# Optimization experiments

Hardware: AMD Instinct MI355X
Metric: run time of the kernel (lower is better)

The kernel has to match this reference:

```python
import jax, jax.numpy as jnp
import numpy as np

N_NODES = 100000
N_EDGES = 1600000
IN_CH = 128
HID = 64
OUT_CH = 10
N_GRAPHS = 64
NEG_SLOPE = 0.2   # GATv2Conv default negative_slope
EPS = 1e-16       # PyG softmax eps


def setup_inputs() -> dict:
    key = jax.random.key(0)
    ks = jax.random.split(key, 10)
    x = jax.random.normal(ks[0], (N_NODES, IN_CH), dtype=jnp.float32)
    edge_index = jax.random.randint(ks[1], (2, N_EDGES), 0, N_NODES, dtype=jnp.int64)
    batch = jnp.sort(jax.random.randint(ks[2], (N_NODES,), 0, N_GRAPHS, dtype=jnp.int64))
    s = 1.0 / np.sqrt(IN_CH)
    Wl = jax.random.uniform(ks[3], (IN_CH, HID), jnp.float32, -s, s)   # lin_l (source)
    Wr = jax.random.uniform(ks[4], (IN_CH, HID), jnp.float32, -s, s)   # lin_r (target)
    att = jax.random.uniform(ks[5], (HID,), jnp.float32, -1.0 / np.sqrt(HID), 1.0 / np.sqrt(HID))
    bias = jnp.zeros((HID,), jnp.float32)
    sf = 1.0 / np.sqrt(HID)
    fc_w = jax.random.uniform(ks[6], (HID, OUT_CH), jnp.float32, -sf, sf)
    fc_b = jax.random.uniform(ks[7], (OUT_CH,), jnp.float32, -sf, sf)
    return {"x": x, "Wl": Wl, "Wr": Wr, "att": att, "bias": bias,
            "fc_w": fc_w, "fc_b": fc_b, "edge_index": edge_index, "batch": batch}


def reference(x, Wl, Wr, att, bias, fc_w, fc_b, edge_index, batch):
    src, tgt = edge_index[0], edge_index[1]
    # GATv2Conv, heads=1: separate linear for source/target
    xl = x @ Wl                         # [N, H] messages (source side)
    xr = x @ Wr                         # [N, H] target side
    z = xl[src] + xr[tgt]               # [E, H]
    e = jnp.where(z > 0, z, NEG_SLOPE * z) @ att   # [E]
    # segment softmax over incoming edges of each target node
    m = jax.ops.segment_max(e, tgt, num_segments=N_NODES)      # [N]
    a = jnp.exp(e - m[tgt])                                    # [E]
    denom = jax.ops.segment_sum(a, tgt, num_segments=N_NODES)  # [N]
    alpha = a / (denom[tgt] + EPS)                             # [E]
    out = jax.ops.segment_sum(alpha[:, None] * xl[src], tgt, num_segments=N_NODES)
    out = out + bias                                           # [N, H]
    # global mean pool over graphs
    cnt = jax.ops.segment_sum(jnp.ones((N_NODES,), out.dtype), batch, num_segments=N_GRAPHS)
    pooled = jax.ops.segment_sum(out, batch, num_segments=N_GRAPHS) / jnp.maximum(cnt, 1.0)[:, None]
    h = jnp.where(pooled > 0, pooled, 0.01 * pooled)           # F.leaky_relu default slope
    # dropout is identity in eval / p=0
    return h @ fc_w + fc_b                                     # [G, OUT_CH]
```

## Files before the change

kernel.cpp:

```cpp
#include <hip/hip_runtime.h>
#include <hip/hip_bf16.h>

#define NN 100000
#define EE 1600000
#define CIN 128
#define HID 64
#define NG 64
#define NOUT 10
#define BSZ 32
#define NB 3125
#define NBA 3136
#define CAP 768
#define NBC 196
#define CCAP 9216

typedef short s16x8 __attribute__((ext_vector_type(8)));
typedef float f32x4 __attribute__((ext_vector_type(4)));

__device__ __forceinline__ unsigned short f2b(float f) {
  unsigned int b = __float_as_uint(f);
  return (unsigned short)((b + 0x7FFFu + ((b >> 16) & 1u)) >> 16);
}
__device__ __forceinline__ float b2f(unsigned short h) {
  return __uint_as_float(((unsigned int)h) << 16);
}

__global__ __launch_bounds__(256) void k_prep(const float* __restrict__ Wl,
                                              const float* __restrict__ Wr,
                                              unsigned short* __restrict__ Wt) {
  int flat = blockIdx.x * 2048 + threadIdx.x;
  for (int i = 0; i < 8; ++i, flat += 256) {
    int n = flat & 127, k = flat >> 7;
    float v = (n < 64) ? Wl[k * 64 + n] : Wr[k * 64 + (n - 64)];
    Wt[n * 128 + k] = f2b(v);
  }
}

__global__ __launch_bounds__(256) void k_gemm(
    const float* __restrict__ x, const unsigned short* __restrict__ Wt,
    unsigned short* __restrict__ xl, unsigned short* __restrict__ xr) {
  __shared__ unsigned short A[128 * 128];
  __shared__ unsigned short B[128 * 128];
  const int tid = threadIdx.x;
  const int lane = tid & 63;
  const int w = tid >> 6;
  const int nb = blockIdx.x * 128;

  {
    int u = tid;
#pragma unroll
    for (int i = 0; i < 8; ++i, u += 256) {
      int n = u >> 4, slot = u & 15;
      uint4 v = *(const uint4*)((const char*)Wt + u * 16);
      int addr = n * 256 + ((slot * 16) ^ ((n & 7) << 4));
      *(uint4*)((char*)B + addr) = v;
    }
  }
  {
    int f = tid;
#pragma unroll
    for (int i = 0; i < 16; ++i, f += 256) {
      int row = f >> 5, c4 = f & 31;
      int node = nb + row;
      float4 v = make_float4(0.f, 0.f, 0.f, 0.f);
      if (node < NN) v = *(const float4*)(x + (long)node * CIN + c4 * 4);
      uint2 p;
      p.x = (unsigned)f2b(v.x) | ((unsigned)f2b(v.y) << 16);
      p.y = (unsigned)f2b(v.z) | ((unsigned)f2b(v.w) << 16);
      int base16 = row * 256 + (((c4 >> 1) << 4) ^ ((row & 7) << 4));
      *(uint2*)((char*)A + base16 + (c4 & 1) * 8) = p;
    }
  }
  __syncthreads();

  const int m0 = w * 32;
  f32x4 acc[2][8];
#pragma unroll
  for (int mt = 0; mt < 2; ++mt)
#pragma unroll
    for (int nt = 0; nt < 8; ++nt) acc[mt][nt] = (f32x4){0.f, 0.f, 0.f, 0.f};

#pragma unroll
  for (int ks = 0; ks < 4; ++ks) {
    const int kb2 = (ks * 32 + (lane >> 4) * 8) * 2;
    const int r0 = m0 + (lane & 15);
    const int r1 = r0 + 16;
    s16x8 a0 = *(const s16x8*)((char*)A + r0 * 256 + (kb2 ^ ((r0 & 7) << 4)));
    s16x8 a1 = *(const s16x8*)((char*)A + r1 * 256 + (kb2 ^ ((r1 & 7) << 4)));
#pragma unroll
    for (int nt = 0; nt < 8; ++nt) {
      const int col = nt * 16 + (lane & 15);
      s16x8 b =
          *(const s16x8*)((char*)B + col * 256 + (kb2 ^ ((col & 7) << 4)));
      acc[0][nt] =
          __builtin_amdgcn_mfma_f32_16x16x32_bf16(a0, b, acc[0][nt], 0, 0, 0);
      acc[1][nt] =
          __builtin_amdgcn_mfma_f32_16x16x32_bf16(a1, b, acc[1][nt], 0, 0, 0);
    }
  }
  __syncthreads();

#pragma unroll
  for (int mt = 0; mt < 2; ++mt) {
    const int rowb = m0 + mt * 16 + (lane >> 4) * 4;
#pragma unroll
    for (int nt = 0; nt < 8; ++nt) {
      const int col = nt * 16 + (lane & 15);
#pragma unroll
      for (int r = 0; r < 4; ++r)
        *((unsigned short*)A + (rowb + r) * 128 + col) = f2b(acc[mt][nt][r]);
    }
  }
  __syncthreads();

  {
    int u = tid;
#pragma unroll
    for (int i = 0; i < 8; ++i, u += 256) {
      int row = u >> 4, slot = u & 15;
      int node = nb + row;
      if (node < NN) {
        uint4 v = *(const uint4*)((const char*)A + row * 256 + slot * 16);
        if (slot < 8)
          *(uint4*)((char*)xl + (long)node * 128 + slot * 16) = v;
        else
          *(uint4*)((char*)xr + (long)node * 128 + (slot - 8) * 16) = v;
      }
    }
  }
}

__global__ __launch_bounds__(256) void k_coarse(const int* __restrict__ ei,
                                                int* __restrict__ gcurc,
                                                unsigned int* __restrict__ coarse) {
  __shared__ int hist[NBC], lbase[NBC], cur[NBC];
  const int tid = threadIdx.x;
  const int base = blockIdx.x * 4096;
  for (int b = tid; b < NBC; b += 256) hist[b] = 0;
  __syncthreads();
#pragma unroll
  for (int i = 0; i < 16; ++i) {
    int j = base + i * 256 + tid;
    if (j < EE) atomicAdd(&hist[ei[EE + j] >> 9], 1);
  }
  __syncthreads();
  for (int b = tid; b < NBC; b += 256) {
    int c = hist[b];
    lbase[b] = c ? atomicAdd(gcurc + b, c) : 0;
    cur[b] = 0;
  }
  __syncthreads();
#pragma unroll
  for (int i = 0; i < 16; ++i) {
    int j = base + i * 256 + tid;
    if (j < EE) {
      int s = ei[j];
      int t = ei[EE + j];
      int cb = t >> 9;
      int p = lbase[cb] + atomicAdd(&cur[cb], 1);
      if (p < CCAP)
        coarse[(long)cb * CCAP + p] = ((unsigned)s << 9) | (unsigned)(t & 511);
    }
  }
}

__global__ __launch_bounds__(256) void k_fine(
    const int* __restrict__ gcurc, const unsigned int* __restrict__ coarse,
    unsigned int* __restrict__ buckets, unsigned short* __restrict__ sc16,
    int* __restrict__ gcnt) {
  __shared__ unsigned int staged[CCAP];
  __shared__ int hist[512], sc[512], cur[512];
  __shared__ int ex32[16], csum[4], coffs[4];
  const int tid = threadIdx.x;
  const int c = blockIdx.x;
  const int ecnt = min(gcurc[c], CCAP);

  for (int i = tid; i < 512; i += 256) hist[i] = 0;
  __syncthreads();
  for (int i = tid; i < ecnt; i += 256) {
    unsigned v = coarse[(long)c * CCAP + i];
    staged[i] = v;
    atomicAdd(&hist[v & 511u], 1);
  }
  __syncthreads();

  {
    const int w = tid >> 6, lane = tid & 63;
    const int iA = w * 128 + lane, iB = iA + 64;
    int sA = hist[iA], sB = hist[iB];
#pragma unroll
    for (int off = 1; off < 64; off <<= 1) {
      int t1 = __shfl_up(sA, off, 64);
      int t2 = __shfl_up(sB, off, 64);
      if (lane >= off) { sA += t1; sB += t2; }
    }
    int tA = __shfl(sA, 63, 64);
    int tB = __shfl(sB, 63, 64);
    sc[iA] = sA;
    sc[iB] = sB + tA;
    if (lane == 0) csum[w] = tA + tB;
    __syncthreads();
    if (tid == 0) {
      int r = 0;
#pragma unroll
      for (int q = 0; q < 4; ++q) { coffs[q] = r; r += csum[q]; }
    }
    __syncthreads();
    sc[iA] += coffs[w];
    sc[iB] += coffs[w];
  }
  __syncthreads();

  if (tid < 16) ex32[tid] = sc[tid * 32] - hist[tid * 32];
  __syncthreads();
  for (int i = tid; i < 512; i += 256) {
    int f = i >> 5;
    int ex = sc[i] - hist[i];
    cur[i] = ex;
    int rel = ex - ex32[f];
    if (rel > CAP) rel = CAP;
    sc16[((long)c * 16 + f) * 32 + (i & 31)] = (unsigned short)rel;
  }
  if (tid < 16) {
    int fb = sc[tid * 32 + 31] - ex32[tid];
    gcnt[c * 16 + tid] = fb > CAP ? CAP : fb;
  }
  __syncthreads();
  for (int i = tid; i < ecnt; i += 256) {
    unsigned v = staged[i];
    int t9 = v & 511u;
    int p = atomicAdd(&cur[t9], 1);
    int rel = p - ex32[t9 >> 5];
    if (rel < CAP)
      buckets[((long)c * 16 + (t9 >> 5)) * CAP + rel] = v >> 9;
  }
}

__global__ __launch_bounds__(256) void k_pull2(
    const int* __restrict__ gcnt, const unsigned int* __restrict__ buckets,
    const unsigned short* __restrict__ sc16,
    const unsigned short* __restrict__ xl,
    const unsigned short* __restrict__ xr, const float* __restrict__ att,
    const float* __restrict__ bias, const int* __restrict__ batch,
    float* __restrict__ pooled, float* __restrict__ cnt) {
  __shared__ float pool2[2][HID];
  __shared__ float cnt2[2];
  const int tid = threadIdx.x;
  const int b = blockIdx.x;
  const int t0 = b << 5;
  if (tid < 2 * HID) ((float*)pool2)[tid] = 0.f;
  if (tid < 2) cnt2[tid] = 0.f;
  __syncthreads();

  const int g = tid & 15;
  const int grp = tid >> 4;
  const float4 a4 = *(const float4*)(att + g * 4);
  const float4 b4 = *(const float4*)(bias + g * 4);
  const int g0 = batch[t0];

#pragma unroll
  for (int rep = 0; rep < 2; ++rep) {
    const int d = grp * 2 + rep;
    const int n = t0 + d;
    const ushort4 ut = *(const ushort4*)(xr + (long)n * HID + g * 4);
    const float xtx = b2f(ut.x), xty = b2f(ut.y);
    const float xtz = b2f(ut.z), xtw = b2f(ut.w);
    float4 acc = make_float4(0.f, 0.f, 0.f, 0.f);
    float den = 0.f;
    const int e0 = sc16[(long)b * 32 + d];
    const int e1 = (d < 31) ? (int)sc16[(long)b * 32 + d + 1] : gcnt[b];
    int e = e0;
    for (; e + 1 < e1; e += 2) {
      const int s0 = buckets[(long)b * CAP + e];
      const int s1 = buckets[(long)b * CAP + e + 1];
      const ushort4 u0 = *(const ushort4*)(xl + (long)s0 * HID + g * 4);
      const ushort4 u1 = *(const ushort4*)(xl + (long)s1 * HID + g * 4);
      const float x0x = b2f(u0.x), x0y = b2f(u0.y);
      const float x0z = b2f(u0.z), x0w = b2f(u0.w);
      const float x1x = b2f(u1.x), x1y = b2f(u1.y);
      const float x1z = b2f(u1.z), x1w = b2f(u1.w);
      float zx0 = x0x + xtx, zy0 = x0y + xty, zz0 = x0z + xtz, zw0 = x0w + xtw;
      float zx1 = x1x + xtx, zy1 = x1y + xty, zz1 = x1z + xtz, zw1 = x1w + xtw;
      zx0 = zx0 > 0.f ? zx0 : 0.2f * zx0;
      zy0 = zy0 > 0.f ? zy0 : 0.2f * zy0;
      zz0 = zz0 > 0.f ? zz0 : 0.2f * zz0;
      zw0 = zw0 > 0.f ? zw0 : 0.2f * zw0;
      zx1 = zx1 > 0.f ? zx1 : 0.2f * zx1;
      zy1 = zy1 > 0.f ? zy1 : 0.2f * zy1;
      zz1 = zz1 > 0.f ? zz1 : 0.2f * zz1;
      zw1 = zw1 > 0.f ? zw1 : 0.2f * zw1;
      float p0 = zx0 * a4.x + zy0 * a4.y + zz0 * a4.z + zw0 * a4.w;
      float p1 = zx1 * a4.x + zy1 * a4.y + zz1 * a4.z + zw1 * a4.w;
      p0 += __shfl_xor(p0, 1, 16);
      p1 += __shfl_xor(p1, 1, 16);
      p0 += __shfl_xor(p0, 2, 16);
      p1 += __shfl_xor(p1, 2, 16);
      p0 += __shfl_xor(p0, 4, 16);
      p1 += __shfl_xor(p1, 4, 16);
      p0 += __shfl_xor(p0, 8, 16);
      p1 += __shfl_xor(p1, 8, 16);
      const float a0 = __expf(p0);
      const float a1 = __expf(p1);
      den += a0 + a1;
      acc.x = fmaf(a0, x0x, acc.x);
      acc.y = fmaf(a0, x0y, acc.y);
      acc.z = fmaf(a0, x0z, acc.z);
      acc.w = fmaf(a0, x0w, acc.w);
      acc.x = fmaf(a1, x1x, acc.x);
      acc.y = fmaf(a1, x1y, acc.y);
      acc.z = fmaf(a1, x1z, acc.z);
      acc.w = fmaf(a1, x1w, acc.w);
    }
    if (e < e1) {
      const int s0 = buckets[(long)b * CAP + e];
      const ushort4 u0 = *(const ushort4*)(xl + (long)s0 * HID + g * 4);
      const float x0x = b2f(u0.x), x0y = b2f(u0.y);
      const float x0z = b2f(u0.z), x0w = b2f(u0.w);
      float zx0 = x0x + xtx, zy0 = x0y + xty, zz0 = x0z + xtz, zw0 = x0w + xtw;
      zx0 = zx0 > 0.f ? zx0 : 0.2f * zx0;
      zy0 = zy0 > 0.f ? zy0 : 0.2f * zy0;
      zz0 = zz0 > 0.f ? zz0 : 0.2f * zz0;
      zw0 = zw0 > 0.f ? zw0 : 0.2f * zw0;
      float p0 = zx0 * a4.x + zy0 * a4.y + zz0 * a4.z + zw0 * a4.w;
      p0 += __shfl_xor(p0, 1, 16);
      p0 += __shfl_xor(p0, 2, 16);
      p0 += __shfl_xor(p0, 4, 16);
      p0 += __shfl_xor(p0, 8, 16);
      const float a0 = __expf(p0);
      den += a0;
      acc.x = fmaf(a0, x0x, acc.x);
      acc.y = fmaf(a0, x0y, acc.y);
      acc.z = fmaf(a0, x0z, acc.z);
      acc.w = fmaf(a0, x0w, acc.w);
    }
    const float inv = 1.f / (den + 1e-16f);
    float4 v4 = make_float4(fmaf(acc.x, inv, b4.x), fmaf(acc.y, inv, b4.y),
                            fmaf(acc.z, inv, b4.z), fmaf(acc.w, inv, b4.w));
    const int gr = batch[n];
    const int idx = gr - g0;
    if (idx >= 0 && idx < 2) {
      atomicAdd(&pool2[idx][g * 4 + 0], v4.x);
      atomicAdd(&pool2[idx][g * 4 + 1], v4.y);
      atomicAdd(&pool2[idx][g * 4 + 2], v4.z);
      atomicAdd(&pool2[idx][g * 4 + 3], v4.w);
      if (g == 0) atomicAdd(&cnt2[idx], 1.f);
    } else {
      atomicAdd(pooled + gr * HID + g * 4 + 0, v4.x);
      atomicAdd(pooled + gr * HID + g * 4 + 1, v4.y);
      atomicAdd(pooled + gr * HID + g * 4 + 2, v4.z);
      atomicAdd(pooled + gr * HID + g * 4 + 3, v4.w);
      if (g == 0) atomicAdd(cnt + gr, 1.f);
    }
  }
  __syncthreads();
  if (tid < 2 * HID) {
    const int which = tid >> 6, c = tid & 63;
    const int gg = g0 + which;
    const float val = pool2[which][c];
    if (gg < NG && val != 0.f) atomicAdd(pooled + gg * HID + c, val);
  }
  if (tid < 2) {
    const int gg = g0 + tid;
    if (gg < NG && cnt2[tid] != 0.f) atomicAdd(cnt + gg, cnt2[tid]);
  }
}

__global__ void k_final(const float* __restrict__ pooled,
                        const float* __restrict__ cnt,
                        const float* __restrict__ fc_w,
                        const float* __restrict__ fc_b,
                        float* __restrict__ out) {
  const int tid = threadIdx.x;
  if (tid >= NG * NOUT) return;
  const int gr = tid / NOUT, o = tid % NOUT;
  const float cg = fmaxf(cnt[gr], 1.0f);
  float acc = fc_b[o];
#pragma unroll 8
  for (int h = 0; h < HID; ++h) {
    float pv = pooled[gr * HID + h] / cg;
    float hv = pv > 0.f ? pv : 0.01f * pv;
    acc = fmaf(hv, fc_w[h * NOUT + o], acc);
  }
  out[gr * NOUT + o] = acc;
}

extern "C" void kernel_launch(void* const* d_in, const int* in_sizes, int n_in,
                              void* d_out, int out_size, void* d_ws,
                              size_t ws_size, hipStream_t stream) {
  const float* x = (const float*)d_in[0];
  const float* Wl = (const float*)d_in[1];
  const float* Wr = (const float*)d_in[2];
  const float* att = (const float*)d_in[3];
  const float* bias = (const float*)d_in[4];
  const float* fc_w = (const float*)d_in[5];
  const float* fc_b = (const float*)d_in[6];
  const int* ei = (const int*)d_in[7];
  const int* batch = (const int*)d_in[8];
  float* out = (float*)d_out;

  char* w = (char*)d_ws;
  unsigned short* xl = (unsigned short*)w;            w += (long)NN * HID * 2;
  unsigned short* xr = (unsigned short*)w;            w += (long)NN * HID * 2;
  unsigned short* Wt = (unsigned short*)w;            w += 128 * 128 * 2;
  unsigned int* coarse = (unsigned int*)w;            w += (long)NBC * CCAP * 4;
  unsigned int* buckets = (unsigned int*)w;           w += (long)NBA * CAP * 4;
  unsigned short* sc16 = (unsigned short*)w;          w += (long)NBA * 32 * 2;
  int* gcnt = (int*)w;                                w += NBA * 4;
  int* gcurc = (int*)w;                               w += NBC * 4;
  float* pooled = (float*)w;                          w += NG * HID * 4;
  float* cnt = (float*)w;                             w += NG * 4;

  hipMemsetAsync(gcurc, 0, (size_t)(NBC + NG * HID + NG) * sizeof(int),
                 stream);

  k_prep<<<8, 256, 0, stream>>>(Wl, Wr, Wt);
  k_gemm<<<(NN + 127) / 128, 256, 0, stream>>>(x, Wt, xl, xr);
  k_coarse<<<(EE + 4095) / 4096, 256, 0, stream>>>(ei, gcurc, coarse);
  k_fine<<<NBC, 256, 0, stream>>>(gcurc, coarse, buckets, sc16, gcnt);
  k_pull2<<<NB, 256, 0, stream>>>(gcnt, buckets, sc16, xl, xr, att, bias,
                                  batch, pooled, cnt);
  k_final<<<1, NG * NOUT, 0, stream>>>(pooled, cnt, fc_w, fc_b, out);
}
```

Before: 255.1 us.

## Map 8 lanes per target node in pull kernel, preload edges in coarse scatter

The pull kernel now assigns 8 lanes per destination node, each holding 8 channels loaded with one 16-byte read, instead of 16 lanes handling 4 channels over two sequential nodes. This widens the gather loads, shortens the shuffle reduction by one step, and lets all 32 nodes of a block proceed at once. The coarse bucketing kernel loads each edge's source and target into registers once and reuses them for both the histogram and scatter passes, avoiding a second global read. The cost is higher register pressure from the 8-wide arrays and 16-entry edge buffers.

```diff
diff --git a/kernel.cpp b/kernel.cpp
--- a/kernel.cpp
+++ b/kernel.cpp
@@ -21,8 +21,11 @@
   unsigned int b = __float_as_uint(f);
   return (unsigned short)((b + 0x7FFFu + ((b >> 16) & 1u)) >> 16);
 }
-__device__ __forceinline__ float b2f(unsigned short h) {
-  return __uint_as_float(((unsigned int)h) << 16);
+__device__ __forceinline__ float b2f_lo(unsigned int u) {
+  return __uint_as_float(u << 16);
+}
+__device__ __forceinline__ float b2f_hi(unsigned int u) {
+  return __uint_as_float(u & 0xFFFF0000u);
 }
 
 __global__ __launch_bounds__(256) void k_prep(const float* __restrict__ Wl,
@@ -136,13 +139,22 @@
   __shared__ int hist[NBC], lbase[NBC], cur[NBC];
   const int tid = threadIdx.x;
   const int base = blockIdx.x * 4096;
+  int ss[16], tt[16];
   for (int b = tid; b < NBC; b += 256) hist[b] = 0;
-  __syncthreads();
 #pragma unroll
   for (int i = 0; i < 16; ++i) {
     int j = base + i * 256 + tid;
-    if (j < EE) atomicAdd(&hist[ei[EE + j] >> 9], 1);
-  }
+    if (j < EE) {
+      ss[i] = ei[j];
+      tt[i] = ei[EE + j];
+    } else {
+      tt[i] = -1;
+    }
+  }
+  __syncthreads();
+#pragma unroll
+  for (int i = 0; i < 16; ++i)
+    if (tt[i] >= 0) atomicAdd(&hist[tt[i] >> 9], 1);
   __syncthreads();
   for (int b = tid; b < NBC; b += 256) {
     int c = hist[b];
@@ -152,14 +164,12 @@
   __syncthreads();
 #pragma unroll
   for (int i = 0; i < 16; ++i) {
-    int j = base + i * 256 + tid;
-    if (j < EE) {
-      int s = ei[j];
-      int t = ei[EE + j];
-      int cb = t >> 9;
+    if (tt[i] >= 0) {
+      int cb = tt[i] >> 9;
       int p = lbase[cb] + atomicAdd(&cur[cb], 1);
       if (p < CCAP)
-        coarse[(long)cb * CCAP + p] = ((unsigned)s << 9) | (unsigned)(t & 511);
+        coarse[(long)cb * CCAP + p] =
+            ((unsigned)ss[i] << 9) | (unsigned)(tt[i] & 511);
     }
   }
 }
@@ -252,107 +262,115 @@
   if (tid < 2) cnt2[tid] = 0.f;
   __syncthreads();
 
-  const int g = tid & 15;
-  const int grp = tid >> 4;
-  const float4 a4 = *(const float4*)(att + g * 4);
-  const float4 b4 = *(const float4*)(bias + g * 4);
+  const int l8 = tid & 7;
+  const int d = tid >> 3;
+  const int n = t0 + d;
+  float av[8];
+  {
+    float4 alo = *(const float4*)(att + l8 * 8);
+    float4 ahi = *(const float4*)(att + l8 * 8 + 4);
+    av[0] = alo.x; av[1] = alo.y; av[2] = alo.z; av[3] = alo.w;
+    av[4] = ahi.x; av[5] = ahi.y; av[6] = ahi.z; av[7] = ahi.w;
+  }
+  float xt[8];
+  {
+    uint4 ur = *(const uint4*)(xr + (long)n * HID + l8 * 8);
+    xt[0] = b2f_lo(ur.x); xt[1] = b2f_hi(ur.x);
+    xt[2] = b2f_lo(ur.y); xt[3] = b2f_hi(ur.y);
+    xt[4] = b2f_lo(ur.z); xt[5] = b2f_hi(ur.z);
+    xt[6] = b2f_lo(ur.w); xt[7] = b2f_hi(ur.w);
+  }
+  float acc[8] = {0.f, 0.f, 0.f, 0.f, 0.f, 0.f, 0.f, 0.f};
+  float den = 0.f;
+  const int e0 = sc16[(long)b * 32 + d];
+  const int e1 = (d < 31) ? (int)sc16[(long)b * 32 + d + 1] : gcnt[b];
+  const unsigned int* brow = buckets + (long)b * CAP;
+  int e = e0;
+  for (; e + 1 < e1; e += 2) {
+    const int s0 = brow[e];
+    const int s1 = brow[e + 1];
+    const uint4 u0 = *(const uint4*)(xl + (long)s0 * HID + l8 * 8);
+    const uint4 u1 = *(const uint4*)(xl + (long)s1 * HID + l8 * 8);
+    float x0[8], x1[8];
+    x0[0] = b2f_lo(u0.x); x0[1] = b2f_hi(u0.x);
+    x0[2] = b2f_lo(u0.y); x0[3] = b2f_hi(u0.y);
+    x0[4] = b2f_lo(u0.z); x0[5] = b2f_hi(u0.z);
+    x0[6] = b2f_lo(u0.w); x0[7] = b2f_hi(u0.w);
+    x1[0] = b2f_lo(u1.x); x1[1] = b2f_hi(u1.x);
+    x1[2] = b2f_lo(u1.y); x1[3] = b2f_hi(u1.y);
+    x1[4] = b2f_lo(u1.z); x1[5] = b2f_hi(u1.z);
+    x1[6] = b2f_lo(u1.w); x1[7] = b2f_hi(u1.w);
+    float p0 = 0.f, p1 = 0.f;
+#pragma unroll
+    for (int c = 0; c < 8; ++c) {
+      float z0 = x0[c] + xt[c];
+      float z1 = x1[c] + xt[c];
+      z0 = z0 > 0.f ? z0 : 0.2f * z0;
+      z1 = z1 > 0.f ? z1 : 0.2f * z1;
+      p0 = fmaf(z0, av[c], p0);
+      p1 = fmaf(z1, av[c], p1);
+    }
+    p0 += __shfl_xor(p0, 1, 8);
+    p1 += __shfl_xor(p1, 1, 8);
+    p0 += __shfl_xor(p0, 2, 8);
+    p1 += __shfl_xor(p1, 2, 8);
+    p0 += __shfl_xor(p0, 4, 8);
+    p1 += __shfl_xor(p1, 4, 8);
+    const float a0 = __expf(p0);
+    const float a1 = __expf(p1);
+    den += a0 + a1;
+#pragma unroll
+    for (int c = 0; c < 8; ++c) {
+      acc[c] = fmaf(a0, x0[c], acc[c]);
+      acc[c] = fmaf(a1, x1[c], acc[c]);
+    }
+  }
+  if (e < e1) {
+    const int s0 = brow[e];
+    const uint4 u0 = *(const uint4*)(xl + (long)s0 * HID + l8 * 8);
+    float x0[8];
+    x0[0] = b2f_lo(u0.x); x0[1] = b2f_hi(u0.x);
+    x0[2] = b2f_lo(u0.y); x0[3] = b2f_hi(u0.y);
+    x0[4] = b2f_lo(u0.z); x0[5] = b2f_hi(u0.z);
+    x0[6] = b2f_lo(u0.w); x0[7] = b2f_hi(u0.w);
+    float p0 = 0.f;
+#pragma unroll
+    for (int c = 0; c < 8; ++c) {
+      float z0 = x0[c] + xt[c];
+      z0 = z0 > 0.f ? z0 : 0.2f * z0;
+      p0 = fmaf(z0, av[c], p0);
+    }
+    p0 += __shfl_xor(p0, 1, 8);
+    p0 += __shfl_xor(p0, 2, 8);
+    p0 += __shfl_xor(p0, 4, 8);
+    const float a0 = __expf(p0);
+    den += a0;
+#pragma unroll
+    for (int c = 0; c < 8; ++c) acc[c] = fmaf(a0, x0[c], acc[c]);
+  }
+  const float inv = 1.f / (den + 1e-16f);
+  const int gr = batch[n];
+  const int idx = gr - batch[t0];
+  float bv[8];
+  {
+    float4 blo = *(const float4*)(bias + l8 * 8);
+    float4 bhi = *(const float4*)(bias + l8 * 8 + 4);
+    bv[0] = blo.x; bv[1] = blo.y; bv[2] = blo.z; bv[3] = blo.w;
+    bv[4] = bhi.x; bv[5] = bhi.y; bv[6] = bhi.z; bv[7] = bhi.w;
+  }
+  if (idx >= 0 && idx < 2) {
+#pragma unroll
+    for (int c = 0; c < 8; ++c)
+      atomicAdd(&pool2[idx][l8 * 8 + c], fmaf(acc[c], inv, bv[c]));
+    if (l8 == 0) atomicAdd(&cnt2[idx], 1.f);
+  } else {
+#pragma unroll
+    for (int c = 0; c < 8; ++c)
+      atomicAdd(pooled + gr * HID + l8 * 8 + c, fmaf(acc[c], inv, bv[c]));
+    if (l8 == 0) atomicAdd(cnt + gr, 1.f);
+  }
+  __syncthreads();
   const int g0 = batch[t0];
-
-#pragma unroll
-  for (int rep = 0; rep < 2; ++rep) {
-    const int d = grp * 2 + rep;
-    const int n = t0 + d;
-    const ushort4 ut = *(const ushort4*)(xr + (long)n * HID + g * 4);
-    const float xtx = b2f(ut.x), xty = b2f(ut.y);
-    const float xtz = b2f(ut.z), xtw = b2f(ut.w);
-    float4 acc = make_float4(0.f, 0.f, 0.f, 0.f);
-    float den = 0.f;
-    const int e0 = sc16[(long)b * 32 + d];
-    const int e1 = (d < 31) ? (int)sc16[(long)b * 32 + d + 1] : gcnt[b];
-    int e = e0;
-    for (; e + 1 < e1; e += 2) {
-      const int s0 = buckets[(long)b * CAP + e];
-      const int s1 = buckets[(long)b * CAP + e + 1];
-      const ushort4 u0 = *(const ushort4*)(xl + (long)s0 * HID + g * 4);
-      const ushort4 u1 = *(const ushort4*)(xl + (long)s1 * HID + g * 4);
-      const float x0x = b2f(u0.x), x0y = b2f(u0.y);
-      const float x0z = b2f(u0.z), x0w = b2f(u0.w);
-      const float x1x = b2f(u1.x), x1y = b2f(u1.y);
-      const float x1z = b2f(u1.z), x1w = b2f(u1.w);
-      float zx0 = x0x + xtx, zy0 = x0y + xty, zz0 = x0z + xtz, zw0 = x0w + xtw;
-      float zx1 = x1x + xtx, zy1 = x1y + xty, zz1 = x1z + xtz, zw1 = x1w + xtw;
-      zx0 = zx0 > 0.f ? zx0 : 0.2f * zx0;
-      zy0 = zy0 > 0.f ? zy0 : 0.2f * zy0;
-      zz0 = zz0 > 0.f ? zz0 : 0.2f * zz0;
-      zw0 = zw0 > 0.f ? zw0 : 0.2f * zw0;
-      zx1 = zx1 > 0.f ? zx1 : 0.2f * zx1;
-      zy1 = zy1 > 0.f ? zy1 : 0.2f * zy1;
-      zz1 = zz1 > 0.f ? zz1 : 0.2f * zz1;
-      zw1 = zw1 > 0.f ? zw1 : 0.2f * zw1;
-      float p0 = zx0 * a4.x + zy0 * a4.y + zz0 * a4.z + zw0 * a4.w;
-      float p1 = zx1 * a4.x + zy1 * a4.y + zz1 * a4.z + zw1 * a4.w;
-      p0 += __shfl_xor(p0, 1, 16);
-      p1 += __shfl_xor(p1, 1, 16);
-      p0 += __shfl_xor(p0, 2, 16);
-      p1 += __shfl_xor(p1, 2, 16);
-      p0 += __shfl_xor(p0, 4, 16);
-      p1 += __shfl_xor(p1, 4, 16);
-      p0 += __shfl_xor(p0, 8, 16);
-      p1 += __shfl_xor(p1, 8, 16);
-      const float a0 = __expf(p0);
-      const float a1 = __expf(p1);
-      den += a0 + a1;
-      acc.x = fmaf(a0, x0x, acc.x);
-      acc.y = fmaf(a0, x0y, acc.y);
-      acc.z = fmaf(a0, x0z, acc.z);
-      acc.w = fmaf(a0, x0w, acc.w);
-      acc.x = fmaf(a1, x1x, acc.x);
-      acc.y = fmaf(a1, x1y, acc.y);
-      acc.z = fmaf(a1, x1z, acc.z);
-      acc.w = fmaf(a1, x1w, acc.w);
-    }
-    if (e < e1) {
-      const int s0 = buckets[(long)b * CAP + e];
-      const ushort4 u0 = *(const ushort4*)(xl + (long)s0 * HID + g * 4);
-      const float x0x = b2f(u0.x), x0y = b2f(u0.y);
-      const float x0z = b2f(u0.z), x0w = b2f(u0.w);
-      float zx0 = x0x + xtx, zy0 = x0y + xty, zz0 = x0z + xtz, zw0 = x0w + xtw;
-      zx0 = zx0 > 0.f ? zx0 : 0.2f * zx0;
-      zy0 = zy0 > 0.f ? zy0 : 0.2f * zy0;
-      zz0 = zz0 > 0.f ? zz0 : 0.2f * zz0;
-      zw0 = zw0 > 0.f ? zw0 : 0.2f * zw0;
-      float p0 = zx0 * a4.x + zy0 * a4.y + zz0 * a4.z + zw0 * a4.w;
-      p0 += __shfl_xor(p0, 1, 16);
-      p0 += __shfl_xor(p0, 2, 16);
-      p0 += __shfl_xor(p0, 4, 16);
-      p0 += __shfl_xor(p0, 8, 16);
-      const float a0 = __expf(p0);
-      den += a0;
-      acc.x = fmaf(a0, x0x, acc.x);
-      acc.y = fmaf(a0, x0y, acc.y);
-      acc.z = fmaf(a0, x0z, acc.z);
-      acc.w = fmaf(a0, x0w, acc.w);
-    }
-    const float inv = 1.f / (den + 1e-16f);
-    float4 v4 = make_float4(fmaf(acc.x, inv, b4.x), fmaf(acc.y, inv, b4.y),
-                            fmaf(acc.z, inv, b4.z), fmaf(acc.w, inv, b4.w));
-    const int gr = batch[n];
-    const int idx = gr - g0;
-    if (idx >= 0 && idx < 2) {
-      atomicAdd(&pool2[idx][g * 4 + 0], v4.x);
-      atomicAdd(&pool2[idx][g * 4 + 1], v4.y);
-      atomicAdd(&pool2[idx][g * 4 + 2], v4.z);
-      atomicAdd(&pool2[idx][g * 4 + 3], v4.w);
-      if (g == 0) atomicAdd(&cnt2[idx], 1.f);
-    } else {
-      atomicAdd(pooled + gr * HID + g * 4 + 0, v4.x);
-      atomicAdd(pooled + gr * HID + g * 4 + 1, v4.y);
-      atomicAdd(pooled + gr * HID + g * 4 + 2, v4.z);
-      atomicAdd(pooled + gr * HID + g * 4 + 3, v4.w);
-      if (g == 0) atomicAdd(cnt + gr, 1.f);
-    }
-  }
-  __syncthreads();
   if (tid < 2 * HID) {
     const int which = tid >> 6, c = tid & 63;
     const int gg = g0 + which;
```

Result: faster. 239.5 us (-6.1%).
